# Kernel tuning notes

Measured on AMD Instinct MI355X. Metric: run time of the kernel, lower is better.

Reference implementation:

```python
import jax, jax.numpy as jnp
import numpy as np

K_RATIO = 0.5  # module's k (keep ratio)


def setup_inputs() -> dict:
    key = jax.random.key(0)
    k1, k2 = jax.random.split(key)
    h = jax.random.normal(k1, (8, 4096, 512), dtype=jnp.float32)
    adj = jax.random.uniform(k2, (8, 4096, 4096), dtype=jnp.float32)
    return {"h": h, "adj": adj}


def reference(h, adj):
    B, N, D = h.shape
    K = max(1, int(K_RATIO * N))
    # scores_i = sum_j <Z_i, Z_j> == <Z_i, sum_j Z_j>  (p=0 so Z == h).
    # Algebraically identical to bmm(Z, Z^T).sum(-1) but O(N*D) not O(N^2*D).
    col_sum = jnp.sum(h, axis=1)                       # [B, D]
    scores = jnp.einsum('bnd,bd->bn', h, col_sum)      # [B, N]
    # topk with largest=False -> K smallest scores, then sort indices ascending.
    _, idx = jax.lax.top_k(-scores, K)                 # [B, K]
    idx = jnp.sort(idx, axis=1)
    # Gather kept node features and kept adjacency rows (permute=False path).
    new_h = jnp.take_along_axis(h, idx[:, :, None], axis=1)     # [B, K, D]
    new_adj = jnp.take_along_axis(adj, idx[:, :, None], axis=1)  # [B, K, N]
    return new_h, new_adj
```

## Files before the change

### kernel.cpp

```cpp
#include <hip/hip_runtime.h>

#define BATCH 8
#define NN 4096
#define DD 512
#define KK 2048
#define NCHUNK 32
#define ROWS_PER_CHUNK (NN / NCHUNK)
#define SPLIT 16
#define JSPLIT 8
#define JCH (NN / JSPLIT)
#define ADJ_UNITS (BATCH * KK)
#define H_UNITS (BATCH * KK * (DD / 4) / 256)
#define GATHER_GRID 2048

typedef float v4f __attribute__((ext_vector_type(4)));

__global__ __launch_bounds__(512) void colsum_partial_kernel(
    const float* __restrict__ h, double* __restrict__ partial) {
    int b = blockIdx.x / NCHUNK;
    int c = blockIdx.x % NCHUNK;
    int c4 = threadIdx.x & 127;
    int rr = threadIdx.x >> 7;
    const float4* hp = (const float4*)h +
        ((size_t)(b * NN + c * ROWS_PER_CHUNK)) * (DD / 4) + c4;
    double a0 = 0, a1 = 0, a2 = 0, a3 = 0;
    #pragma unroll 4
    for (int n = rr; n < ROWS_PER_CHUNK; n += 4) {
        float4 v = hp[(size_t)n * (DD / 4)];
        a0 += v.x; a1 += v.y; a2 += v.z; a3 += v.w;
    }
    double* pp = partial + (((size_t)(b * NCHUNK + c) * 4 + rr) * DD) + c4 * 4;
    pp[0] = a0; pp[1] = a1; pp[2] = a2; pp[3] = a3;
}

__global__ __launch_bounds__(512) void colsum_reduce_kernel(
    const double* __restrict__ partial, double* __restrict__ colsum) {
    int b = blockIdx.x;
    int d = threadIdx.x;
    double acc = 0.0;
    #pragma unroll 8
    for (int q = 0; q < NCHUNK * 4; ++q)
        acc += partial[((size_t)b * NCHUNK * 4 + q) * DD + d];
    colsum[b * DD + d] = acc;
}

__global__ __launch_bounds__(256) void scores_kernel(
    const float* __restrict__ h, const double* __restrict__ colsum,
    float* __restrict__ scores) {
    int wave = threadIdx.x >> 6;
    int lane = threadIdx.x & 63;
    int r = blockIdx.x * 4 + wave;
    int b = r >> 12;
    const float4* hp = (const float4*)(h + (size_t)r * DD) + lane * 2;
    float4 v0 = hp[0];
    float4 v1 = hp[1];
    const double* cs = colsum + b * DD + lane * 8;
    double acc = (double)v0.x * cs[0] + (double)v0.y * cs[1] +
                 (double)v0.z * cs[2] + (double)v0.w * cs[3] +
                 (double)v1.x * cs[4] + (double)v1.y * cs[5] +
                 (double)v1.z * cs[6] + (double)v1.w * cs[7];
    #pragma unroll
    for (int off = 32; off >= 1; off >>= 1) acc += __shfl_down(acc, off);
    if (lane == 0) scores[r] = (float)acc;
}

__global__ __launch_bounds__(256) void count_kernel(
    const float* __restrict__ scores, int* __restrict__ pcount) {
    __shared__ float sc[JCH];
    int blk = blockIdx.x;
    int jc = blk % JSPLIT;
    int s  = (blk / JSPLIT) % SPLIT;
    int b  = blk / (JSPLIT * SPLIT);
    const float* srow = scores + b * NN;
    for (int j = threadIdx.x; j < JCH; j += 256) sc[j] = srow[jc * JCH + j];
    __syncthreads();
    int i = s * 256 + threadIdx.x;
    float si = srow[i];
    int jbase = jc * JCH;
    int cnt = 0;
    const float4* sc4 = (const float4*)sc;
    #pragma unroll 4
    for (int jj = 0; jj < JCH / 4; ++jj) {
        float4 sv = sc4[jj];
        int j0 = jbase + jj * 4;
        cnt += (sv.x < si || (sv.x == si && (j0 + 0) < i)) ? 1 : 0;
        cnt += (sv.y < si || (sv.y == si && (j0 + 1) < i)) ? 1 : 0;
        cnt += (sv.z < si || (sv.z == si && (j0 + 2) < i)) ? 1 : 0;
        cnt += (sv.w < si || (sv.w == si && (j0 + 3) < i)) ? 1 : 0;
    }
    pcount[((size_t)jc * BATCH + b) * NN + i] = cnt;
}

__global__ __launch_bounds__(1024) void compact_kernel(
    const int* __restrict__ pcount, int* __restrict__ idx) {
    __shared__ int wtot[16];
    int b = blockIdx.x;
    int t = threadIdx.x;
    int lane = t & 63, w = t >> 6;
    int f[4];
    #pragma unroll
    for (int q = 0; q < 4; ++q) {
        int i = t * 4 + q;
        int cnt = 0;
        #pragma unroll
        for (int jc = 0; jc < JSPLIT; ++jc)
            cnt += pcount[((size_t)jc * BATCH + b) * NN + i];
        f[q] = (cnt < KK) ? 1 : 0;
    }
    int local = f[0] + f[1] + f[2] + f[3];
    int scan = local;
    #pragma unroll
    for (int off = 1; off < 64; off <<= 1) {
        int x = __shfl_up(scan, off);
        if (lane >= off) scan += x;
    }
    if (lane == 63) wtot[w] = scan;
    __syncthreads();
    int wbase = 0;
    for (int ww = 0; ww < w; ++ww) wbase += wtot[ww];
    int p = wbase + scan - local;
    int* irow = idx + b * KK;
    #pragma unroll
    for (int q = 0; q < 4; ++q) {
        if (f[q]) irow[p++] = t * 4 + q;
    }
}

__global__ __launch_bounds__(256) void gather_kernel(
    const float* __restrict__ h, const float* __restrict__ adj,
    const int* __restrict__ idx, float* __restrict__ out_h,
    float* __restrict__ out_adj) {
    for (int u = blockIdx.x; u < ADJ_UNITS + H_UNITS; u += GATHER_GRID) {
        if (u < ADJ_UNITS) {
            int row = u;
            int b = row >> 11;
            int src = idx[row];
            const v4f* ap = (const v4f*)adj + ((size_t)b * NN + src) * (NN / 4);
            v4f* op = (v4f*)out_adj + (size_t)row * (NN / 4);
            #pragma unroll
            for (int q = 0; q < 4; ++q) {
                int v = threadIdx.x + q * 256;
                v4f val = __builtin_nontemporal_load(ap + v);
                __builtin_nontemporal_store(val, op + v);
            }
        } else {
            int tid = (u - ADJ_UNITS) * 256 + threadIdx.x;
            int v = tid & 127;
            int row = tid >> 7;
            int b = row >> 11;
            int src = idx[row];
            v4f val = ((const v4f*)h)[((size_t)b * NN + src) * (DD / 4) + v];
            __builtin_nontemporal_store(val, (v4f*)out_h + tid);
        }
    }
}

extern "C" void kernel_launch(void* const* d_in, const int* in_sizes, int n_in,
                              void* d_out, int out_size, void* d_ws, size_t ws_size,
                              hipStream_t stream) {
    const float* h   = (const float*)d_in[0];
    const float* adj = (const float*)d_in[1];
    float* out = (float*)d_out;
    char* ws = (char*)d_ws;

    double* partial = (double*)ws;
    double* colsum  = (double*)(ws + 4194304);
    float*  scores  = (float*)(ws + 4194304 + 32768);
    int*    pcount  = (int*)(ws + 4194304 + 32768 + 131072);
    int*    idx     = (int*)(ws + 4194304 + 32768 + 131072 + 1048576);

    hipLaunchKernelGGL(colsum_partial_kernel, dim3(BATCH * NCHUNK), dim3(512), 0, stream, h, partial);
    hipLaunchKernelGGL(colsum_reduce_kernel, dim3(BATCH), dim3(512), 0, stream, partial, colsum);
    hipLaunchKernelGGL(scores_kernel, dim3(BATCH * NN / 4), dim3(256), 0, stream, h, colsum, scores);
    hipLaunchKernelGGL(count_kernel, dim3(BATCH * SPLIT * JSPLIT), dim3(256), 0, stream, scores, pcount);
    hipLaunchKernelGGL(compact_kernel, dim3(BATCH), dim3(1024), 0, stream, pcount, idx);
    hipLaunchKernelGGL(gather_kernel, dim3(GATHER_GRID), dim3(256), 0, stream,
                       h, adj, idx, out, out + (size_t)BATCH * KK * DD);
}
```

Baseline: 161.0 us.

## Fuse colsum reduction via atomics and fuse compaction into count kernel

The column-sum now reduces the four row groups in shared memory and adds each block's partial into a zeroed double colsum with atomics, which removes the separate reduce kernel and the partial buffer. The count kernel gains a last-block ticket pattern, so the final block per batch does the prefix-scan compaction with 256 threads each handling 16 nodes. This removes two launches and their gaps but adds a memset, double atomics, and a serial single-block compaction tail per batch. Atomic ordering makes the colsum summation order nondeterministic.

```diff
diff --git a/kernel.cpp b/kernel.cpp
--- a/kernel.cpp
+++ b/kernel.cpp
@@ -5,7 +5,6 @@
 #define DD 512
 #define KK 2048
 #define NCHUNK 32
-#define ROWS_PER_CHUNK (NN / NCHUNK)
 #define SPLIT 16
 #define JSPLIT 8
 #define JCH (NN / JSPLIT)
@@ -15,33 +14,34 @@
 
 typedef float v4f __attribute__((ext_vector_type(4)));
 
-__global__ __launch_bounds__(512) void colsum_partial_kernel(
-    const float* __restrict__ h, double* __restrict__ partial) {
+__global__ __launch_bounds__(512) void colsum_kernel(
+    const float* __restrict__ h, double* __restrict__ colsum) {
+    __shared__ double red[4][DD];
     int b = blockIdx.x / NCHUNK;
     int c = blockIdx.x % NCHUNK;
     int c4 = threadIdx.x & 127;
     int rr = threadIdx.x >> 7;
     const float4* hp = (const float4*)h +
-        ((size_t)(b * NN + c * ROWS_PER_CHUNK)) * (DD / 4) + c4;
+        ((size_t)(b * NN + c * 128)) * (DD / 4) + c4;
     double a0 = 0, a1 = 0, a2 = 0, a3 = 0;
     #pragma unroll 4
-    for (int n = rr; n < ROWS_PER_CHUNK; n += 4) {
+    for (int n = rr; n < 128; n += 4) {
         float4 v = hp[(size_t)n * (DD / 4)];
         a0 += v.x; a1 += v.y; a2 += v.z; a3 += v.w;
     }
-    double* pp = partial + (((size_t)(b * NCHUNK + c) * 4 + rr) * DD) + c4 * 4;
-    pp[0] = a0; pp[1] = a1; pp[2] = a2; pp[3] = a3;
-}
-
-__global__ __launch_bounds__(512) void colsum_reduce_kernel(
-    const double* __restrict__ partial, double* __restrict__ colsum) {
-    int b = blockIdx.x;
-    int d = threadIdx.x;
-    double acc = 0.0;
-    #pragma unroll 8
-    for (int q = 0; q < NCHUNK * 4; ++q)
-        acc += partial[((size_t)b * NCHUNK * 4 + q) * DD + d];
-    colsum[b * DD + d] = acc;
+    red[rr][c4 * 4 + 0] = a0;
+    red[rr][c4 * 4 + 1] = a1;
+    red[rr][c4 * 4 + 2] = a2;
+    red[rr][c4 * 4 + 3] = a3;
+    __syncthreads();
+    if (rr == 0) {
+        #pragma unroll
+        for (int q = 0; q < 4; ++q) {
+            int d = c4 * 4 + q;
+            double s = red[0][d] + red[1][d] + red[2][d] + red[3][d];
+            unsafeAtomicAdd(&colsum[b * DD + d], s);
+        }
+    }
 }
 
 __global__ __launch_bounds__(256) void scores_kernel(
@@ -64,50 +64,60 @@
     if (lane == 0) scores[r] = (float)acc;
 }
 
-__global__ __launch_bounds__(256) void count_kernel(
-    const float* __restrict__ scores, int* __restrict__ pcount) {
+__global__ __launch_bounds__(256) void count_compact_kernel(
+    const float* __restrict__ scores, int* __restrict__ pcount,
+    int* __restrict__ tickets, int* __restrict__ idx) {
     __shared__ float sc[JCH];
+    __shared__ int wtot[4];
+    __shared__ int is_last;
     int blk = blockIdx.x;
     int jc = blk % JSPLIT;
     int s  = (blk / JSPLIT) % SPLIT;
     int b  = blk / (JSPLIT * SPLIT);
+    int t = threadIdx.x;
+
     const float* srow = scores + b * NN;
-    for (int j = threadIdx.x; j < JCH; j += 256) sc[j] = srow[jc * JCH + j];
+    for (int j = t; j < JCH; j += 256) sc[j] = srow[jc * JCH + j];
     __syncthreads();
-    int i = s * 256 + threadIdx.x;
-    float si = srow[i];
-    int jbase = jc * JCH;
-    int cnt = 0;
-    const float4* sc4 = (const float4*)sc;
-    #pragma unroll 4
-    for (int jj = 0; jj < JCH / 4; ++jj) {
-        float4 sv = sc4[jj];
-        int j0 = jbase + jj * 4;
-        cnt += (sv.x < si || (sv.x == si && (j0 + 0) < i)) ? 1 : 0;
-        cnt += (sv.y < si || (sv.y == si && (j0 + 1) < i)) ? 1 : 0;
-        cnt += (sv.z < si || (sv.z == si && (j0 + 2) < i)) ? 1 : 0;
-        cnt += (sv.w < si || (sv.w == si && (j0 + 3) < i)) ? 1 : 0;
+    {
+        int i = s * 256 + t;
+        float si = srow[i];
+        int jbase = jc * JCH;
+        int cnt = 0;
+        const float4* sc4 = (const float4*)sc;
+        #pragma unroll 4
+        for (int jj = 0; jj < JCH / 4; ++jj) {
+            float4 sv = sc4[jj];
+            int j0 = jbase + jj * 4;
+            cnt += (sv.x < si || (sv.x == si && (j0 + 0) < i)) ? 1 : 0;
+            cnt += (sv.y < si || (sv.y == si && (j0 + 1) < i)) ? 1 : 0;
+            cnt += (sv.z < si || (sv.z == si && (j0 + 2) < i)) ? 1 : 0;
+            cnt += (sv.w < si || (sv.w == si && (j0 + 3) < i)) ? 1 : 0;
+        }
+        pcount[((size_t)jc * BATCH + b) * NN + i] = cnt;
     }
-    pcount[((size_t)jc * BATCH + b) * NN + i] = cnt;
-}
+    __threadfence();
+    __syncthreads();
+    if (t == 0) {
+        int old = atomicAdd(&tickets[b], 1);
+        is_last = (old == SPLIT * JSPLIT - 1);
+    }
+    __syncthreads();
+    if (!is_last) return;
 
-__global__ __launch_bounds__(1024) void compact_kernel(
-    const int* __restrict__ pcount, int* __restrict__ idx) {
-    __shared__ int wtot[16];
-    int b = blockIdx.x;
-    int t = threadIdx.x;
+    __threadfence();
     int lane = t & 63, w = t >> 6;
-    int f[4];
+    unsigned mask = 0;
     #pragma unroll
-    for (int q = 0; q < 4; ++q) {
-        int i = t * 4 + q;
+    for (int q = 0; q < 16; ++q) {
+        int i = t * 16 + q;
         int cnt = 0;
         #pragma unroll
-        for (int jc = 0; jc < JSPLIT; ++jc)
-            cnt += pcount[((size_t)jc * BATCH + b) * NN + i];
-        f[q] = (cnt < KK) ? 1 : 0;
+        for (int c = 0; c < JSPLIT; ++c)
+            cnt += pcount[((size_t)c * BATCH + b) * NN + i];
+        if (cnt < KK) mask |= (1u << q);
     }
-    int local = f[0] + f[1] + f[2] + f[3];
+    int local = __popc(mask);
     int scan = local;
     #pragma unroll
     for (int off = 1; off < 64; off <<= 1) {
@@ -121,8 +131,8 @@
     int p = wbase + scan - local;
     int* irow = idx + b * KK;
     #pragma unroll
-    for (int q = 0; q < 4; ++q) {
-        if (f[q]) irow[p++] = t * 4 + q;
+    for (int q = 0; q < 16; ++q) {
+        if ((mask >> q) & 1) irow[p++] = t * 16 + q;
     }
 }
 
@@ -163,17 +173,18 @@
     float* out = (float*)d_out;
     char* ws = (char*)d_ws;
 
-    double* partial = (double*)ws;
-    double* colsum  = (double*)(ws + 4194304);
-    float*  scores  = (float*)(ws + 4194304 + 32768);
-    int*    pcount  = (int*)(ws + 4194304 + 32768 + 131072);
-    int*    idx     = (int*)(ws + 4194304 + 32768 + 131072 + 1048576);
+    double* colsum  = (double*)ws;
+    int*    tickets = (int*)(ws + 32768);
+    float*  scores  = (float*)(ws + 65536);
+    int*    pcount  = (int*)(ws + 65536 + 131072);
+    int*    idx     = (int*)(ws + 65536 + 131072 + 1048576);
 
-    hipLaunchKernelGGL(colsum_partial_kernel, dim3(BATCH * NCHUNK), dim3(512), 0, stream, h, partial);
-    hipLaunchKernelGGL(colsum_reduce_kernel, dim3(BATCH), dim3(512), 0, stream, partial, colsum);
+    hipMemsetAsync(ws, 0, 32768 + 128, stream);
+
+    hipLaunchKernelGGL(colsum_kernel, dim3(BATCH * NCHUNK), dim3(512), 0, stream, h, colsum);
     hipLaunchKernelGGL(scores_kernel, dim3(BATCH * NN / 4), dim3(256), 0, stream, h, colsum, scores);
-    hipLaunchKernelGGL(count_kernel, dim3(BATCH * SPLIT * JSPLIT), dim3(256), 0, stream, scores, pcount);
-    hipLaunchKernelGGL(compact_kernel, dim3(BATCH), dim3(1024), 0, stream, pcount, idx);
+    hipLaunchKernelGGL(count_compact_kernel, dim3(BATCH * SPLIT * JSPLIT), dim3(256), 0, stream,
+                       scores, pcount, tickets, idx);
     hipLaunchKernelGGL(gather_kernel, dim3(GATHER_GRID), dim3(256), 0, stream,
                        h, adj, idx, out, out + (size_t)BATCH * KK * DD);
 }
```

Result: slower. 228.2 us (+41.7%).
